# Kernel optimization log

Hardware: AMD Instinct MI355X
Metric: run time of the kernel (lower is better)

Reference implementation:

```python
import jax, jax.numpy as jnp
import numpy as np

N, E = 40000, 640000
IN_DIM, HID, HEADS, OUT, NC, ASSIGN = 128, 16, 8, 128, 2, 100
SIGMA = 0.5
F_HID = HID * HEADS  # 128 = hidden_dim * n_heads


def _edge_softmax(logits, dst, n):
    # softmax over incoming edges of each destination node (DGL edge_softmax)
    m = jax.ops.segment_max(logits, dst, num_segments=n)
    ex = jnp.exp(logits - m[dst])
    den = jax.ops.segment_sum(ex, dst, num_segments=n)
    return ex / den[dst]


def _gat_conv(h, src, dst, W, al, ar, b):
    # DGL GATConv: fc (no bias) -> per-head additive attention -> edge softmax -> scatter-sum
    nH, D = al.shape
    feat = (h @ W).reshape(h.shape[0], nH, D)            # [N,H,D]
    el = (feat * al).sum(-1)                              # [N,H]
    er = (feat * ar).sum(-1)                              # [N,H]
    logits = jax.nn.leaky_relu(el[src] + er[dst], 0.2)    # [E,H]
    a = _edge_softmax(logits, dst, h.shape[0])            # [E,H]
    out = jax.ops.segment_sum(feat[src] * a[..., None], dst, num_segments=h.shape[0])
    return out + b                                        # [N,H,D]


def _bn(x, g, b, eps=1e-5):
    mu = x.mean(0)
    v = x.var(0)
    return g * (x - mu) * jax.lax.rsqrt(v + eps) + b


def _gat_layer(h, src, dst, W, al, ar, b, g, bt):
    x = _gat_conv(h, src, dst, W, al, ar, b).reshape(h.shape[0], -1)
    x = jax.nn.elu(_bn(x, g, bt))
    return h + x  # residual: in_dim == out_dim*heads


def _mask(x):
    # h[torch.isinf(h)] = 1e9
    return jnp.where(jnp.isinf(x), 1e9, x)


def setup_inputs():
    key = jax.random.key(0)
    ks = jax.random.split(key, 20)
    rn = lambda k, s: jax.random.normal(k, s, jnp.float32) * 0.1
    return {
        "h": jax.random.normal(ks[0], (N, IN_DIM), jnp.float32),
        "e": jax.random.normal(ks[1], (E, 4), jnp.float32),
        "src": jax.random.randint(ks[2], (E,), 0, N, jnp.int32),
        "dst": jax.random.randint(ks[3], (E,), 0, N, jnp.int32),
        "W_emb": rn(ks[4], (IN_DIM, F_HID)), "b_emb": jnp.zeros((F_HID,), jnp.float32),
        "Wg": rn(ks[5], (3, F_HID, F_HID)),
        "alg": rn(ks[6], (3, HEADS, HID)), "arg": rn(ks[7], (3, HEADS, HID)),
        "bg": jnp.zeros((3, HEADS, HID), jnp.float32),
        "gam": jnp.ones((3, F_HID), jnp.float32), "bet": jnp.zeros((3, F_HID), jnp.float32),
        "W3": rn(ks[8], (F_HID, OUT)), "al3": rn(ks[9], (1, OUT)), "ar3": rn(ks[10], (1, OUT)),
        "b3": jnp.zeros((1, OUT), jnp.float32),
        "gam3": jnp.ones((OUT,), jnp.float32), "bet3": jnp.zeros((OUT,), jnp.float32),
        "Wa": rn(ks[11], (F_HID, ASSIGN)), "ba": jnp.zeros((ASSIGN,), jnp.float32),
        "Wm1": rn(ks[12], (2 * OUT, OUT)), "bm1": jnp.zeros((OUT,), jnp.float32),
        "Wm2": rn(ks[13], (OUT, OUT // 2)), "bm2": jnp.zeros((OUT // 2,), jnp.float32),
        "Wm3": rn(ks[14], (OUT // 2, NC)), "bm3": jnp.zeros((NC,), jnp.float32),
    }


def reference(h, e, src, dst, W_emb, b_emb, Wg, alg, arg, bg, gam, bet,
              W3, al3, ar3, b3, gam3, bet3, Wa, ba,
              Wm1, bm1, Wm2, bm2, Wm3, bm3):
    del e  # edge_feat=False: forward never consumes edge features
    h = h @ W_emb + b_emb  # embedding_h (dropout p=0 -> identity)
    # layer 0: GATLayer
    h = _mask(_gat_layer(h, src, dst, Wg[0], alg[0], arg[0], bg[0], gam[0], bet[0]))
    # layer 1: biGATLayer -> (h, s): GAT update + soft assignment s with sigma mixing over coarse pool
    h_in = h
    h_fine = _gat_layer(h, src, dst, Wg[1], alg[1], arg[1], bg[1], gam[1], bet[1])
    s = jax.nn.softmax(h_in @ Wa + ba, axis=-1)            # [N, ASSIGN]
    h_coarse = s.T @ h_fine                                # [ASSIGN, F_HID]
    h = _mask(SIGMA * h_fine + (1.0 - SIGMA) * (s @ h_coarse))
    # layer 2: GATLayer
    h = _mask(_gat_layer(h, src, dst, Wg[2], alg[2], arg[2], bg[2], gam[2], bet[2]))
    # layer 3: GATLayer, 1 head, out_dim
    h = _mask(_gat_layer(h, src, dst, W3, al3, ar3, b3, gam3, bet3))
    # apply_edges: gather src/dst node feats, concat, MLPReadout (256->128->64->NC), inf-mask
    z = jnp.concatenate([h[src], h[dst]], axis=1)          # [E, 2*OUT]
    z = jax.nn.relu(z @ Wm1 + bm1)
    z = jax.nn.relu(z @ Wm2 + bm2)
    z = _mask(z @ Wm3 + bm3)
    return z, s
```

## Files before the change

kernel.cpp:

```cpp
#include <hip/hip_runtime.h>
#include <hip/hip_bf16.h>
#include <math.h>

#define N_ 40000
#define E_ 640000
#define CB_ 400
#define CR_ 100
#define SB_ 256
#define SNB_ 157
#define AGGB_ 2048

typedef short bf16x8 __attribute__((ext_vector_type(8)));
typedef float floatx4 __attribute__((ext_vector_type(4)));

__device__ __forceinline__ short f2bf(float f) {
    __hip_bfloat16 h = __float2bfloat16(f);
    return *reinterpret_cast<short*>(&h);
}
__device__ __forceinline__ float bf2f(short u) {
    unsigned int x = ((unsigned int)(unsigned short)u) << 16;
    return __int_as_float(x);
}
__device__ __forceinline__ float rdlane(float v, int l) {
    return __int_as_float(__builtin_amdgcn_readlane(__float_as_int(v), l));
}
__device__ __forceinline__ float bflo(unsigned int u) { return __int_as_float(u << 16); }
__device__ __forceinline__ float bfhi(unsigned int u) { return __int_as_float(u & 0xffff0000u); }

__global__ void k_count(const int* __restrict__ dst, int* __restrict__ counts) {
    for (int e = blockIdx.x * blockDim.x + threadIdx.x; e < E_; e += gridDim.x * blockDim.x)
        atomicAdd(&counts[dst[e]], 1);
}

__global__ __launch_bounds__(256) void k_scanA(const int* __restrict__ counts,
                                               int* __restrict__ excl,
                                               int* __restrict__ bsum) {
    int t = threadIdx.x;
    int i = blockIdx.x * SB_ + t;
    int v = (i < N_) ? counts[i] : 0;
    int lane = t & 63, wv = t >> 6;
    int x = v;
#pragma unroll
    for (int off = 1; off < 64; off <<= 1) {
        int y = __shfl_up(x, off);
        if (lane >= off) x += y;
    }
    __shared__ int wsum[4];
    __shared__ int woff[4];
    if (lane == 63) wsum[wv] = x;
    __syncthreads();
    if (t == 0) {
        int a = 0;
#pragma unroll
        for (int j = 0; j < 4; j++) { int tv = wsum[j]; woff[j] = a; a += tv; }
        bsum[blockIdx.x] = a;
    }
    __syncthreads();
    if (i < N_) excl[i] = x - v + woff[wv];
}

__global__ __launch_bounds__(256) void k_scanB(int* __restrict__ bsum) {
    int t = threadIdx.x;
    int v = (t < SNB_) ? bsum[t] : 0;
    int lane = t & 63, wv = t >> 6;
    int x = v;
#pragma unroll
    for (int off = 1; off < 64; off <<= 1) {
        int y = __shfl_up(x, off);
        if (lane >= off) x += y;
    }
    __shared__ int wsum[4];
    __shared__ int woff[4];
    if (lane == 63) wsum[wv] = x;
    __syncthreads();
    if (t == 0) {
        int a = 0;
#pragma unroll
        for (int j = 0; j < 4; j++) { int tv = wsum[j]; woff[j] = a; a += tv; }
    }
    __syncthreads();
    if (t < SNB_) bsum[t] = x - v + woff[wv];
}

__global__ __launch_bounds__(256) void k_scanC(const int* __restrict__ excl,
                                               const int* __restrict__ bsum,
                                               int* __restrict__ rowptr,
                                               int* __restrict__ cursor) {
    int i = blockIdx.x * 256 + threadIdx.x;
    if (i < N_) {
        int r = excl[i] + bsum[i / SB_];
        rowptr[i] = r;
        cursor[i] = r;
    }
    if (i == N_) rowptr[N_] = E_;
}

__global__ void k_fill(const int* __restrict__ src, const int* __restrict__ dst,
                       int* __restrict__ cursor, int* __restrict__ srcv,
                       unsigned short* __restrict__ dstv, int* __restrict__ eidv) {
    for (int e = blockIdx.x * blockDim.x + threadIdx.x; e < E_; e += gridDim.x * blockDim.x) {
        int d = dst[e];
        int pos = atomicAdd(&cursor[d], 1);
        srcv[pos] = src[e];
        dstv[pos] = (unsigned short)d;
        eidv[pos] = e;
    }
}

__global__ __launch_bounds__(256) void k_prep_all(const float* __restrict__ Wg,
                                                  const float* __restrict__ W3,
                                                  const float* __restrict__ Wm1,
                                                  short* __restrict__ WbT6) {
    int i = blockIdx.x * 256 + threadIdx.x;
    if (i >= 6 * 16384) return;
    int m = i >> 14;
    int r = i & 16383;
    int n = r >> 7, k = r & 127;
    const float* srcp;
    switch (m) {
        case 0: srcp = Wg; break;
        case 1: srcp = Wg + 16384; break;
        case 2: srcp = Wg + 32768; break;
        case 3: srcp = W3; break;
        case 4: srcp = Wm1; break;
        default: srcp = Wm1 + 16384; break;
    }
    WbT6[m * 16384 + n * 128 + k] = f2bf(srcp[k * 128 + n]);
}

__global__ __launch_bounds__(256) void k_prep_wela(const float* __restrict__ Wg,
                                                   const float* __restrict__ alg,
                                                   const float* __restrict__ arg_,
                                                   const float* __restrict__ W3,
                                                   const float* __restrict__ al3,
                                                   const float* __restrict__ ar3,
                                                   short* __restrict__ WelT) {
    int i = blockIdx.x * 256 + threadIdx.x;
    if (i >= 4 * 2048) return;
    int layer = i >> 11;
    int r = i & 2047;
    int n = r >> 7, k = r & 127;
    float val = 0.f;
    if (layer < 3) {
        const float* W = Wg + layer * 16384;
        const float* a = (n < 8 ? alg : arg_) + layer * 128;
        int h = n & 7;
#pragma unroll
        for (int d = 0; d < 16; d++)
            val += W[k * 128 + h * 16 + d] * a[h * 16 + d];
    } else {
        if (n == 0) { for (int c = 0; c < 128; c++) val += W3[k * 128 + c] * al3[c]; }
        else if (n == 1) { for (int c = 0; c < 128; c++) val += W3[k * 128 + c] * ar3[c]; }
    }
    WelT[layer * 2048 + n * 128 + k] = f2bf(val);
}

__global__ __launch_bounds__(256) void k_prep_hilo(const float* __restrict__ W_emb,
                                                   const float* __restrict__ Wa,
                                                   short* __restrict__ WembT_hi,
                                                   short* __restrict__ WembT_lo,
                                                   short* __restrict__ WaT_hi,
                                                   short* __restrict__ WaT_lo) {
    int i = blockIdx.x * 256 + threadIdx.x;
    if (i >= 2 * 16384) return;
    int m = i >> 14;
    int r = i & 16383;
    int n = r >> 7, k = r & 127;
    if (m == 0) {
        float w = W_emb[k * 128 + n];
        short h = f2bf(w);
        WembT_hi[n * 128 + k] = h;
        WembT_lo[n * 128 + k] = f2bf(w - bf2f(h));
    } else {
        float w = (n < 100) ? Wa[k * 100 + n] : 0.f;
        short h = f2bf(w);
        WaT_hi[n * 128 + k] = h;
        WaT_lo[n * 128 + k] = f2bf(w - bf2f(h));
    }
}

__global__ __launch_bounds__(256) void k_mfma_hilo(const float* __restrict__ A,
                                                   const short* __restrict__ BT_hi,
                                                   const short* __restrict__ BT_lo,
                                                   const float* __restrict__ bias,
                                                   float* __restrict__ C, int ncols) {
    __shared__ short sAh[64 * 136];
    __shared__ short sAl[64 * 136];
    __shared__ short sBh[128 * 136];
    int t = threadIdx.x;
    int r0 = blockIdx.x * 64;
    {
        int n = t >> 1;
        int k0 = (t & 1) * 64;
#pragma unroll
        for (int j = 0; j < 8; j++) {
            bf16x8 v = *(const bf16x8*)(BT_hi + n * 128 + k0 + 8 * j);
            *(bf16x8*)(sBh + n * 136 + k0 + 8 * j) = v;
        }
    }
    {
        int r = t >> 2;
        int k0 = (t & 3) * 32;
        const float* ar = A + (size_t)(r0 + r) * 128 + k0;
#pragma unroll
        for (int j = 0; j < 4; j++) {
            float4 f0 = *(const float4*)(ar + 8 * j);
            float4 f1 = *(const float4*)(ar + 8 * j + 4);
            float x[8] = {f0.x, f0.y, f0.z, f0.w, f1.x, f1.y, f1.z, f1.w};
            bf16x8 vh, vl;
#pragma unroll
            for (int q = 0; q < 8; q++) {
                short hh = f2bf(x[q]);
                vh[q] = hh;
                vl[q] = f2bf(x[q] - bf2f(hh));
            }
            *(bf16x8*)(sAh + r * 136 + k0 + 8 * j) = vh;
            *(bf16x8*)(sAl + r * 136 + k0 + 8 * j) = vl;
        }
    }
    __syncthreads();
    int lane = t & 63, wv = t >> 6;
    int lm = lane & 15, quad = lane >> 4;
    int m0 = wv * 16;
    bf16x8 aH[4], aL[4];
#pragma unroll
    for (int kt = 0; kt < 4; kt++) {
        aH[kt] = *(const bf16x8*)(sAh + (m0 + lm) * 136 + kt * 32 + quad * 8);
        aL[kt] = *(const bf16x8*)(sAl + (m0 + lm) * 136 + kt * 32 + quad * 8);
    }
#pragma unroll
    for (int nt = 0; nt < 8; nt++) {
        const short* blp = BT_lo + (nt * 16 + lm) * 128 + quad * 8;
        floatx4 acc = (floatx4){0.f, 0.f, 0.f, 0.f};
#pragma unroll
        for (int kt = 0; kt < 4; kt++) {
            bf16x8 bH = *(const bf16x8*)(sBh + (nt * 16 + lm) * 136 + kt * 32 + quad * 8);
            bf16x8 bL = *(const bf16x8*)(blp + kt * 32);
            acc = __builtin_amdgcn_mfma_f32_16x16x32_bf16(aH[kt], bH, acc, 0, 0, 0);
            acc = __builtin_amdgcn_mfma_f32_16x16x32_bf16(aL[kt], bH, acc, 0, 0, 0);
            acc = __builtin_amdgcn_mfma_f32_16x16x32_bf16(aH[kt], bL, acc, 0, 0, 0);
        }
        int col = nt * 16 + lm;
        if (col < ncols) {
            float bv = bias ? bias[col] : 0.f;
#pragma unroll
            for (int r = 0; r < 4; r++) {
                int row = r0 + m0 + quad * 4 + r;
                C[(size_t)row * ncols + col] = acc[r] + bv;
            }
        }
    }
}

__global__ __launch_bounds__(256) void k_gemm_mfma(const float* __restrict__ A,
                                                   const short* __restrict__ WbT,
                                                   const float* __restrict__ bias,
                                                   short* __restrict__ C,
                                                   const short* __restrict__ WelT,
                                                   float* __restrict__ el,
                                                   float* __restrict__ er,
                                                   int H,
                                                   const float* __restrict__ bnx,
                                                   const float* __restrict__ bnh,
                                                   const float* __restrict__ csum,
                                                   const float* __restrict__ csq,
                                                   const float* __restrict__ bng,
                                                   const float* __restrict__ bnb,
                                                   float* __restrict__ hout,
                                                   int do_mask,
                                                   const short* __restrict__ WbT2,
                                                   short* __restrict__ C2) {
    __shared__ short sA[64 * 136];
    __shared__ short sB[128 * 136];
    __shared__ float sScale[128];
    __shared__ float sShift[128];
    int t = threadIdx.x;
    int r0 = blockIdx.x * 64;
    if (bnx) {
        if (t < 128) {
            const float invN = 1.f / (float)N_;
            float mu = csum[t] * invN;
            float var = csq[t] * invN - mu * mu;
            float inv = rsqrtf(var + 1e-5f);
            float sc = bng[t] * inv;
            sScale[t] = sc;
            sShift[t] = bnb[t] - mu * sc;
        }
        __syncthreads();
    }
    {
        int n = t >> 1;
        int k0 = (t & 1) * 64;
#pragma unroll
        for (int j = 0; j < 8; j++) {
            bf16x8 v = *(const bf16x8*)(WbT + n * 128 + k0 + 8 * j);
            *(bf16x8*)(sB + n * 136 + k0 + 8 * j) = v;
        }
    }
    {
        int r = t >> 2;
        int k0 = (t & 3) * 32;
        if (bnx) {
            const float* xr = bnx + (size_t)(r0 + r) * 128 + k0;
            const float* hr = bnh + (size_t)(r0 + r) * 128 + k0;
            float* ho = hout + (size_t)(r0 + r) * 128 + k0;
#pragma unroll
            for (int j = 0; j < 4; j++) {
                float4 x0 = *(const float4*)(xr + 8 * j);
                float4 x1 = *(const float4*)(xr + 8 * j + 4);
                float4 h0 = *(const float4*)(hr + 8 * j);
                float4 h1 = *(const float4*)(hr + 8 * j + 4);
                float xs[8] = {x0.x, x0.y, x0.z, x0.w, x1.x, x1.y, x1.z, x1.w};
                float hs[8] = {h0.x, h0.y, h0.z, h0.w, h1.x, h1.y, h1.z, h1.w};
                float ov[8];
                bf16x8 v;
#pragma unroll
                for (int q = 0; q < 8; q++) {
                    int c = k0 + 8 * j + q;
                    float y = sScale[c] * xs[q] + sShift[c];
                    y = y > 0.f ? y : (__expf(y) - 1.f);
                    float hv = hs[q] + y;
                    if (do_mask && isinf(hv)) hv = 1e9f;
                    ov[q] = hv;
                    v[q] = f2bf(hv);
                }
                *(float4*)(ho + 8 * j) = make_float4(ov[0], ov[1], ov[2], ov[3]);
                *(float4*)(ho + 8 * j + 4) = make_float4(ov[4], ov[5], ov[6], ov[7]);
                *(bf16x8*)(sA + r * 136 + k0 + 8 * j) = v;
            }
        } else {
            const float* ar = A + (size_t)(r0 + r) * 128 + k0;
#pragma unroll
            for (int j = 0; j < 4; j++) {
                float4 f0 = *(const float4*)(ar + 8 * j);
                float4 f1 = *(const float4*)(ar + 8 * j + 4);
                bf16x8 v;
                v[0] = f2bf(f0.x); v[1] = f2bf(f0.y); v[2] = f2bf(f0.z); v[3] = f2bf(f0.w);
                v[4] = f2bf(f1.x); v[5] = f2bf(f1.y); v[6] = f2bf(f1.z); v[7] = f2bf(f1.w);
                *(bf16x8*)(sA + r * 136 + k0 + 8 * j) = v;
            }
        }
    }
    __syncthreads();
    int lane = t & 63, wv = t >> 6;
    int lm = lane & 15, quad = lane >> 4;
    int m0 = wv * 16;
    bf16x8 aF[4];
#pragma unroll
    for (int kt = 0; kt < 4; kt++)
        aF[kt] = *(const bf16x8*)(sA + (m0 + lm) * 136 + kt * 32 + quad * 8);
#pragma unroll
    for (int nt = 0; nt < 8; nt++) {
        floatx4 acc = (floatx4){0.f, 0.f, 0.f, 0.f};
#pragma unroll
        for (int kt = 0; kt < 4; kt++) {
            bf16x8 bF = *(const bf16x8*)(sB + (nt * 16 + lm) * 136 + kt * 32 + quad * 8);
            acc = __builtin_amdgcn_mfma_f32_16x16x32_bf16(aF[kt], bF, acc, 0, 0, 0);
        }
        int col = nt * 16 + lm;
        float bv = bias ? bias[col] : 0.f;
#pragma unroll
        for (int r = 0; r < 4; r++) {
            int row = r0 + m0 + quad * 4 + r;
            C[(size_t)row * 128 + col] = f2bf(acc[r] + bv);
        }
    }
    if (WelT) {
        floatx4 acc = (floatx4){0.f, 0.f, 0.f, 0.f};
#pragma unroll
        for (int kt = 0; kt < 4; kt++) {
            bf16x8 wF = *(const bf16x8*)(WelT + lm * 128 + kt * 32 + quad * 8);
            acc = __builtin_amdgcn_mfma_f32_16x16x32_bf16(aF[kt], wF, acc, 0, 0, 0);
        }
        if (H == 8) {
#pragma unroll
            for (int r = 0; r < 4; r++) {
                int row = r0 + m0 + quad * 4 + r;
                if (lm < 8) el[(size_t)row * 8 + lm] = acc[r];
                else        er[(size_t)row * 8 + (lm - 8)] = acc[r];
            }
        } else {
#pragma unroll
            for (int r = 0; r < 4; r++) {
                int row = r0 + m0 + quad * 4 + r;
                if (lm == 0) el[row] = acc[r];
                if (lm == 1) er[row] = acc[r];
            }
        }
    }
    if (WbT2) {
        __syncthreads();
        {
            int n = t >> 1;
            int k0 = (t & 1) * 64;
#pragma unroll
            for (int j = 0; j < 8; j++) {
                bf16x8 v = *(const bf16x8*)(WbT2 + n * 128 + k0 + 8 * j);
                *(bf16x8*)(sB + n * 136 + k0 + 8 * j) = v;
            }
        }
        __syncthreads();
#pragma unroll
        for (int nt = 0; nt < 8; nt++) {
            floatx4 acc = (floatx4){0.f, 0.f, 0.f, 0.f};
#pragma unroll
            for (int kt = 0; kt < 4; kt++) {
                bf16x8 bF = *(const bf16x8*)(sB + (nt * 16 + lm) * 136 + kt * 32 + quad * 8);
                acc = __builtin_amdgcn_mfma_f32_16x16x32_bf16(aF[kt], bF, acc, 0, 0, 0);
            }
            int col = nt * 16 + lm;
#pragma unroll
            for (int r = 0; r < 4; r++) {
                int row = r0 + m0 + quad * 4 + r;
                C2[(size_t)row * 128 + col] = f2bf(acc[r]);
            }
        }
    }
}

__global__ __launch_bounds__(256) void k_smax100(const float* __restrict__ logits,
                                                 float* __restrict__ s) {
    int lane = threadIdx.x & 63;
    int n = blockIdx.x * 4 + (threadIdx.x >> 6);
    if (n >= N_) return;
    bool act = lane < 50;
    float2 v = make_float2(-INFINITY, -INFINITY);
    if (act) v = *(const float2*)(logits + (size_t)n * 100 + 2 * lane);
    float mx = fmaxf(v.x, v.y);
#pragma unroll
    for (int off = 1; off < 64; off <<= 1) mx = fmaxf(mx, __shfl_xor(mx, off));
    float e0 = act ? __expf(v.x - mx) : 0.f;
    float e1 = act ? __expf(v.y - mx) : 0.f;
    float sm = e0 + e1;
#pragma unroll
    for (int off = 1; off < 64; off <<= 1) sm += __shfl_xor(sm, off);
    float inv = 1.f / sm;
    if (act) *(float2*)(s + (size_t)n * 100 + 2 * lane) = make_float2(e0 * inv, e1 * inv);
}

template <int H>
__global__ __launch_bounds__(256) void k_gat_agg(const short* __restrict__ feat,
                                                 const float* __restrict__ el,
                                                 const float* __restrict__ er,
                                                 const int* __restrict__ rowptr,
                                                 const int* __restrict__ srcv,
                                                 const float* __restrict__ bias,
                                                 float* __restrict__ xout,
                                                 float* __restrict__ psum,
                                                 float* __restrict__ psq) {
    int t = threadIdx.x;
    int lane = t & 63;
    int gw = (blockIdx.x * blockDim.x + t) >> 6;
    int nw = (gridDim.x * blockDim.x) >> 6;
    constexpr int LH = (H == 8) ? 3 : 0;
    int h = lane & (H - 1);
    int f0 = 2 * lane;
    int hf = (H == 8) ? (lane >> 3) : 0;

    float stx = 0.f, sty = 0.f, qtx = 0.f, qty = 0.f;

    for (int n = gw; n < N_; n += nw) {
        int beg = rowptr[n], end = rowptr[n + 1];
        if (beg == end) {
            float2 b2 = *(const float2*)(bias + f0);
            *(float2*)(xout + (size_t)n * 128 + f0) = b2;
            stx += b2.x; sty += b2.y;
            qtx += b2.x * b2.x; qty += b2.y * b2.y;
            continue;
        }
        float ern = er[(size_t)n * H + h];
        float m = -INFINITY, ss = 0.f;
        for (int e = beg + (lane >> LH); e < end; e += (64 >> LH)) {
            int sI = srcv[e];
            float x = el[(size_t)sI * H + h] + ern;
            float lr = x > 0.f ? x : 0.2f * x;
            if (lr > m) { ss = ss * __expf(m - lr) + 1.f; m = lr; }
            else ss += __expf(lr - m);
        }
#pragma unroll
        for (int off = H; off < 64; off <<= 1) {
            float om = __shfl_xor(m, off);
            float os = __shfl_xor(ss, off);
            float nm = fmaxf(m, om);
            float p1 = (m == -INFINITY) ? 0.f : ss * __expf(m - nm);
            float p2 = (om == -INFINITY) ? 0.f : os * __expf(om - nm);
            m = nm; ss = p1 + p2;
        }
        float inv_d = 1.f / ss;
        int endm1 = end - 1;
        float accx = 0.f, accy = 0.f;
        for (int e0 = beg; e0 < end; e0 += 16) {
            int le = lane >> 3;
            int eLA = e0 + le, eLB = e0 + 8 + le;
            int eCA = eLA <= endm1 ? eLA : endm1;
            int eCB = eLB <= endm1 ? eLB : endm1;
            int sLA = srcv[eCA];
            int sLB = srcv[eCB];
            float xA = el[(size_t)sLA * H + h] + ern;
            float xB = el[(size_t)sLB * H + h] + ern;
            float lrA = xA > 0.f ? xA : 0.2f * xA;
            float lrB = xB > 0.f ? xB : 0.2f * xB;
            float wA = __expf(lrA - m) * inv_d;
            float wB = __expf(lrB - m) * inv_d;
            if (eLA > endm1) wA = 0.f;
            if (eLB > endm1) wB = 0.f;
            bool haveB = (e0 + 8) < end;
            unsigned int uuA[8], uuB[8];
#pragma unroll
            for (int j = 0; j < 8; j++) {
                int sj = __builtin_amdgcn_readlane(sLA, j * 8);
                uuA[j] = *(const unsigned int*)(feat + (size_t)sj * 128 + f0);
            }
            if (haveB) {
#pragma unroll
                for (int j = 0; j < 8; j++) {
                    int sj = __builtin_amdgcn_readlane(sLB, j * 8);
                    uuB[j] = *(const unsigned int*)(feat + (size_t)sj * 128 + f0);
                }
            }
#pragma unroll
            for (int j = 0; j < 8; j++) {
                float aj;
                if (H == 8) aj = __shfl(wA, j * 8 + hf);
                else        aj = rdlane(wA, j * 8);
                accx += aj * bflo(uuA[j]);
                accy += aj * bfhi(uuA[j]);
            }
            if (haveB) {
#pragma unroll
                for (int j = 0; j < 8; j++) {
                    float aj;
                    if (H == 8) aj = __shfl(wB, j * 8 + hf);
                    else        aj = rdlane(wB, j * 8);
                    accx += aj * bflo(uuB[j]);
                    accy += aj * bfhi(uuB[j]);
                }
            }
        }
        float2 b2 = *(const float2*)(bias + f0);
        float ox = accx + b2.x, oy = accy + b2.y;
        *(float2*)(xout + (size_t)n * 128 + f0) = make_float2(ox, oy);
        stx += ox; sty += oy;
        qtx += ox * ox; qty += oy * oy;
    }

    __shared__ float red[4][256];
    red[0][t] = stx; red[1][t] = sty; red[2][t] = qtx; red[3][t] = qty;
    __syncthreads();
    if (t < 64) {
        float a0 = red[0][t] + red[0][t + 64] + red[0][t + 128] + red[0][t + 192];
        float a1 = red[1][t] + red[1][t + 64] + red[1][t + 128] + red[1][t + 192];
        float q0 = red[2][t] + red[2][t + 64] + red[2][t + 128] + red[2][t + 192];
        float q1 = red[3][t] + red[3][t + 64] + red[3][t + 128] + red[3][t + 192];
        *(float2*)(psum + (size_t)blockIdx.x * 128 + 2 * t) = make_float2(a0, a1);
        *(float2*)(psq + (size_t)blockIdx.x * 128 + 2 * t) = make_float2(q0, q1);
    }
}

__global__ __launch_bounds__(256) void k_stats_reduce(const float* __restrict__ psum,
                                                      const float* __restrict__ psq,
                                                      float* __restrict__ colsum,
                                                      float* __restrict__ colsq) {
    __shared__ float ls[256], lq[256];
    int t = threadIdx.x;
    int col = t & 127, half = t >> 7;
    float s = 0.f, q = 0.f;
    for (int b = blockIdx.x * 2 + half; b < AGGB_; b += gridDim.x * 2) {
        s += psum[(size_t)b * 128 + col];
        q += psq[(size_t)b * 128 + col];
    }
    ls[t] = s; lq[t] = q;
    __syncthreads();
    if (t < 128) {
        atomicAdd(&colsum[col], ls[t] + ls[t + 128]);
        atomicAdd(&colsq[col], lq[t] + lq[t + 128]);
    }
}

__global__ __launch_bounds__(256) void k_bn_apply(const float* __restrict__ x,
                                                  const float* __restrict__ hprev,
                                                  const float* __restrict__ sum,
                                                  const float* __restrict__ sumsq,
                                                  const float* __restrict__ g,
                                                  const float* __restrict__ b,
                                                  float* __restrict__ out, int do_mask) {
    int i = blockIdx.x * blockDim.x + threadIdx.x;
    if (i >= N_ * 128) return;
    int c = i & 127;
    const float invN = 1.f / (float)N_;
    float mu = sum[c] * invN;
    float var = sumsq[c] * invN - mu * mu;
    float inv = rsqrtf(var + 1e-5f);
    float y = g[c] * (x[i] - mu) * inv + b[c];
    y = y > 0.f ? y : (__expf(y) - 1.f);
    float hv = hprev[i] + y;
    if (do_mask && isinf(hv)) hv = 1e9f;
    out[i] = hv;
}

__global__ __launch_bounds__(512) void k_coarse_part(const float* __restrict__ s,
                                                     const float* __restrict__ hf,
                                                     float* __restrict__ part) {
    int t = threadIdx.x;
    int c = t & 127;
    int g = t >> 7;
    int lane = t & 63;
    float acc[25];
#pragma unroll
    for (int a = 0; a < 25; a++) acc[a] = 0.f;
    int n0 = blockIdx.x * CR_;
    for (int n = n0; n < n0 + CR_; n += 2) {
        float hv0 = hf[(size_t)n * 128 + c];
        float hv1 = hf[(size_t)(n + 1) * 128 + c];
        float sv0 = 0.f, sv1 = 0.f;
        if (lane < 25) {
            sv0 = s[(size_t)n * 100 + 25 * g + lane];
            sv1 = s[(size_t)(n + 1) * 100 + 25 * g + lane];
        }
#pragma unroll
        for (int a = 0; a < 25; ++a) {
            float a0 = rdlane(sv0, a);
            float a1 = rdlane(sv1, a);
            acc[a] += a0 * hv0 + a1 * hv1;
        }
    }
    float* dstp = part + (size_t)blockIdx.x * 12800 + (size_t)(25 * g) * 128 + c;
#pragma unroll
    for (int a = 0; a < 25; a++) dstp[a * 128] = acc[a];
}

__global__ __launch_bounds__(256) void k_coarse_reduce(const float* __restrict__ part,
                                                       float* __restrict__ hc) {
    int i = blockIdx.x * blockDim.x + threadIdx.x;
    if (i >= 12800) return;
    float s0 = 0.f, s1 = 0.f, s2 = 0.f, s3 = 0.f;
    for (int b = 0; b < CB_; b += 4) {
        s0 += part[(size_t)(b + 0) * 12800 + i];
        s1 += part[(size_t)(b + 1) * 12800 + i];
        s2 += part[(size_t)(b + 2) * 12800 + i];
        s3 += part[(size_t)(b + 3) * 12800 + i];
    }
    hc[i] = (s0 + s1) + (s2 + s3);
}

__global__ __launch_bounds__(256) void k_combine(const float* __restrict__ s,
                                                 const float* __restrict__ hc,
                                                 const float* __restrict__ hfine,
                                                 float* __restrict__ hout) {
    __shared__ float ssh[16 * 100];
    int t = threadIdx.x;
    int n0 = blockIdx.x * 16;
    for (int u = t; u < 1600; u += 256) ssh[u] = s[(size_t)n0 * 100 + u];
    __syncthreads();
    int c = t & 127, g = t >> 7;
    float acc[8];
#pragma unroll
    for (int r = 0; r < 8; r++) acc[r] = 0.f;
    const float* hcp = hc + c;
    for (int a = 0; a < 100; a += 4) {
        float h0 = hcp[(a + 0) * 128];
        float h1 = hcp[(a + 1) * 128];
        float h2 = hcp[(a + 2) * 128];
        float h3 = hcp[(a + 3) * 128];
#pragma unroll
        for (int r = 0; r < 8; r++) {
            float4 sv = *(const float4*)(ssh + (g * 8 + r) * 100 + a);
            acc[r] += sv.x * h0 + sv.y * h1 + sv.z * h2 + sv.w * h3;
        }
    }
#pragma unroll
    for (int r = 0; r < 8; r++) {
        int row = n0 + g * 8 + r;
        float v = 0.5f * hfine[(size_t)row * 128 + c] + 0.5f * acc[r];
        if (isinf(v)) v = 1e9f;
        hout[(size_t)row * 128 + c] = v;
    }
}

__global__ __launch_bounds__(256) void k_prep_w(const float* __restrict__ Wm2,
                                                short* __restrict__ Wm2T) {
    int i = blockIdx.x * blockDim.x + threadIdx.x;
    if (i >= 64 * 128) return;
    int n = i & 63, k = i >> 6;
    Wm2T[n * 128 + k] = f2bf(Wm2[k * 64 + n]);
}

__global__ __launch_bounds__(256) void k_edge_mlp3(const short* __restrict__ Pb,
                                                   const short* __restrict__ Qb,
                                                   const int* __restrict__ srcv,
                                                   const unsigned short* __restrict__ dstv,
                                                   const int* __restrict__ eidv,
                                                   const short* __restrict__ Wm2T,
                                                   const float* __restrict__ bm2,
                                                   const float* __restrict__ Wm3,
                                                   const float* __restrict__ bm3,
                                                   float* __restrict__ zout) {
    __shared__ short sW[64 * 128];
    int t = threadIdx.x;
    for (int u = t; u < 1024; u += 256) {
        int n = u >> 4, k16 = u & 15;
        int phys = (n << 4) | (k16 ^ (n & 15));
        *(bf16x8*)(sW + phys * 8) = *(const bf16x8*)(Wm2T + n * 128 + k16 * 8);
    }
    int lane = t & 63;
    int lm = lane & 15, quad = lane >> 4;
    float bv[4], w30[4], w31[4];
#pragma unroll
    for (int nt = 0; nt < 4; nt++) {
        int n = nt * 16 + lm;
        bv[nt] = bm2[n]; w30[nt] = Wm3[2 * n]; w31[nt] = Wm3[2 * n + 1];
    }
    float b30 = bm3[0], b31 = bm3[1];
    __syncthreads();

    int gw = (blockIdx.x * blockDim.x + t) >> 6;
    int nw = (gridDim.x * blockDim.x) >> 6;

    for (int tile = gw; tile < E_ / 16; tile += nw) {
        int p0 = tile * 16;
        int sI = srcv[p0 + lm];
        int dI = (int)dstv[p0 + lm];
        const short* pr = Pb + (size_t)sI * 128 + quad * 8;
        const short* qr = Qb + (size_t)dI * 128 + quad * 8;
        uint4 pu[4], qu[4];
#pragma unroll
        for (int kt = 0; kt < 4; kt++) {
            pu[kt] = *(const uint4*)(pr + kt * 32);
            qu[kt] = *(const uint4*)(qr + kt * 32);
        }
        bf16x8 aF[4];
#pragma unroll
        for (int kt = 0; kt < 4; kt++) {
            unsigned int pv[4] = {pu[kt].x, pu[kt].y, pu[kt].z, pu[kt].w};
            unsigned int qv[4] = {qu[kt].x, qu[kt].y, qu[kt].z, qu[kt].w};
            union { uint4 u; bf16x8 v; } cv;
            unsigned int rr[4];
#pragma unroll
            for (int j = 0; j < 4; j++) {
                float fl = fmaxf(bflo(pv[j]) + bflo(qv[j]), 0.f);
                float fh = fmaxf(bfhi(pv[j]) + bfhi(qv[j]), 0.f);
                rr[j] = (unsigned int)(unsigned short)f2bf(fl) |
                        ((unsigned int)(unsigned short)f2bf(fh) << 16);
            }
            cv.u.x = rr[0]; cv.u.y = rr[1]; cv.u.z = rr[2]; cv.u.w = rr[3];
            aF[kt] = cv.v;
        }
        float pz0[4] = {0.f, 0.f, 0.f, 0.f};
        float pz1[4] = {0.f, 0.f, 0.f, 0.f};
#pragma unroll
        for (int nt = 0; nt < 4; nt++) {
            floatx4 acc = (floatx4){0.f, 0.f, 0.f, 0.f};
#pragma unroll
            for (int kt = 0; kt < 4; kt++) {
                int phys = ((nt * 16 + lm) << 4) | (((kt << 2) | quad) ^ lm);
                bf16x8 bF = *(const bf16x8*)(sW + phys * 8);
                acc = __builtin_amdgcn_mfma_f32_16x16x32_bf16(aF[kt], bF, acc, 0, 0, 0);
            }
#pragma unroll
            for (int r = 0; r < 4; r++) {
                float u = fmaxf(acc[r] + bv[nt], 0.f);
                pz0[r] += u * w30[nt];
                pz1[r] += u * w31[nt];
            }
        }
#pragma unroll
        for (int off = 1; off < 16; off <<= 1) {
#pragma unroll
            for (int r = 0; r < 4; r++) {
                pz0[r] += __shfl_xor(pz0[r], off);
                pz1[r] += __shfl_xor(pz1[r], off);
            }
        }
        if (lm < 4) {
            int eid = eidv[p0 + quad * 4 + lm];
            float z0 = pz0[lm] + b30;
            float z1 = pz1[lm] + b31;
            if (isinf(z0)) z0 = 1e9f;
            if (isinf(z1)) z1 = 1e9f;
            *(float2*)(zout + (size_t)eid * 2) = make_float2(z0, z1);
        }
    }
}

extern "C" void kernel_launch(void* const* d_in, const int* in_sizes, int n_in,
                              void* d_out, int out_size, void* d_ws, size_t ws_size,
                              hipStream_t stream) {
    const float* h_in  = (const float*)d_in[0];
    const int*   src   = (const int*)d_in[2];
    const int*   dst   = (const int*)d_in[3];
    const float* W_emb = (const float*)d_in[4];
    const float* b_emb = (const float*)d_in[5];
    const float* Wg    = (const float*)d_in[6];
    const float* alg   = (const float*)d_in[7];
    const float* arg_  = (const float*)d_in[8];
    const float* bg    = (const float*)d_in[9];
    const float* gam   = (const float*)d_in[10];
    const float* bet   = (const float*)d_in[11];
    const float* W3    = (const float*)d_in[12];
    const float* al3   = (const float*)d_in[13];
    const float* ar3   = (const float*)d_in[14];
    const float* b3    = (const float*)d_in[15];
    const float* gam3  = (const float*)d_in[16];
    const float* bet3  = (const float*)d_in[17];
    const float* Wa    = (const float*)d_in[18];
    const float* ba    = (const float*)d_in[19];
    const float* Wm1   = (const float*)d_in[20];
    const float* bm1   = (const float*)d_in[21];
    const float* Wm2   = (const float*)d_in[22];
    const float* bm2   = (const float*)d_in[23];
    const float* Wm3   = (const float*)d_in[24];
    const float* bm3   = (const float*)d_in[25];

    float* zout = (float*)d_out;
    float* sout = zout + (size_t)E_ * 2;

    float* ws = (float*)d_ws;
    size_t o = 0;
    float* h_cur = ws + o; o += (size_t)N_ * 128;
    float* xbuf  = ws + o; o += (size_t)N_ * 128;
    float* featb = ws + o; o += (size_t)N_ * 128;
    float* el    = ws + o; o += (size_t)N_ * 8;
    float* er    = ws + o; o += (size_t)N_ * 8;
    float* colsum = ws + o; o += 128;
    float* colsq  = ws + o; o += 128;
    float* hc     = ws + o; o += 100 * 128;
    float* psum   = ws + o; o += (size_t)AGGB_ * 128;
    float* psq    = ws + o; o += (size_t)AGGB_ * 128;
    short* Wm2T = (short*)(ws + o); o += (64 * 128) / 2;
    short* WbT6 = (short*)(ws + o); o += (6 * 16384) / 2;
    short* WelT = (short*)(ws + o); o += (4 * 2048) / 2;
    short* WembT_hi = (short*)(ws + o); o += 16384 / 2;
    short* WembT_lo = (short*)(ws + o); o += 16384 / 2;
    short* WaT_hi   = (short*)(ws + o); o += 16384 / 2;
    short* WaT_lo   = (short*)(ws + o); o += 16384 / 2;
    int* counts = (int*)(ws + o); o += N_;
    int* rowptr = (int*)(ws + o); o += N_ + 4;
    int* cursor = (int*)(ws + o); o += N_;
    int* srcv   = (int*)(ws + o); o += E_;
    unsigned short* dstv = (unsigned short*)(ws + o); o += E_ / 2;
    int* eidv   = (int*)(ws + o); o += E_;
    int* bsum   = (int*)(ws + o); o += SNB_ + 4;

    short* featw = (short*)featb;

    hipMemsetAsync(counts, 0, N_ * sizeof(int), stream);
    k_count<<<1024, 256, 0, stream>>>(dst, counts);
    k_scanA<<<SNB_, 256, 0, stream>>>(counts, eidv, bsum);
    k_scanB<<<1, 256, 0, stream>>>(bsum);
    k_scanC<<<SNB_ + 1, 256, 0, stream>>>(eidv, bsum, rowptr, cursor);
    k_fill<<<1024, 256, 0, stream>>>(src, dst, cursor, srcv, dstv, eidv);
    k_prep_w<<<32, 256, 0, stream>>>(Wm2, Wm2T);
    k_prep_all<<<384, 256, 0, stream>>>(Wg, W3, Wm1, WbT6);
    k_prep_wela<<<32, 256, 0, stream>>>(Wg, alg, arg_, W3, al3, ar3, WelT);
    k_prep_hilo<<<128, 256, 0, stream>>>(W_emb, Wa, WembT_hi, WembT_lo, WaT_hi, WaT_lo);

    k_mfma_hilo<<<N_ / 64, 256, 0, stream>>>(h_in, WembT_hi, WembT_lo, b_emb, h_cur, 128);

    k_gemm_mfma<<<N_ / 64, 256, 0, stream>>>(h_cur, WbT6 + 0 * 16384, nullptr, featw,
                                             WelT + 0 * 2048, el, er, 8,
                                             nullptr, nullptr, nullptr, nullptr,
                                             nullptr, nullptr, nullptr, 0,
                                             nullptr, nullptr);
    hipMemsetAsync(colsum, 0, 256 * sizeof(float), stream);
    k_gat_agg<8><<<AGGB_, 256, 0, stream>>>(featw, el, er, rowptr, srcv, bg + 0 * 128, xbuf,
                                            psum, psq);
    k_stats_reduce<<<64, 256, 0, stream>>>(psum, psq, colsum, colsq);

    k_gemm_mfma<<<N_ / 64, 256, 0, stream>>>(nullptr, WbT6 + 1 * 16384, nullptr, featw,
                                             WelT + 1 * 2048, el, er, 8,
                                             xbuf, h_cur, colsum, colsq,
                                             gam + 0 * 128, bet + 0 * 128, h_cur, 1,
                                             nullptr, nullptr);
    k_mfma_hilo<<<N_ / 64, 256, 0, stream>>>(h_cur, WaT_hi, WaT_lo, ba, xbuf, 100);
    k_smax100<<<N_ / 4, 256, 0, stream>>>(xbuf, sout);
    hipMemsetAsync(colsum, 0, 256 * sizeof(float), stream);
    k_gat_agg<8><<<AGGB_, 256, 0, stream>>>(featw, el, er, rowptr, srcv, bg + 1 * 128, xbuf,
                                            psum, psq);
    k_stats_reduce<<<64, 256, 0, stream>>>(psum, psq, colsum, colsq);
    k_bn_apply<<<(N_ * 128) / 256, 256, 0, stream>>>(xbuf, h_cur, colsum, colsq,
                                                     gam + 1 * 128, bet + 1 * 128, xbuf, 0);
    k_coarse_part<<<CB_, 512, 0, stream>>>(sout, xbuf, featb);
    k_coarse_reduce<<<50, 256, 0, stream>>>(featb, hc);
    k_combine<<<N_ / 16, 256, 0, stream>>>(sout, hc, xbuf, h_cur);

    k_gemm_mfma<<<N_ / 64, 256, 0, stream>>>(h_cur, WbT6 + 2 * 16384, nullptr, featw,
                                             WelT + 2 * 2048, el, er, 8,
                                             nullptr, nullptr, nullptr, nullptr,
                                             nullptr, nullptr, nullptr, 0,
                                             nullptr, nullptr);
    hipMemsetAsync(colsum, 0, 256 * sizeof(float), stream);
    k_gat_agg<8><<<AGGB_, 256, 0, stream>>>(featw, el, er, rowptr, srcv, bg + 2 * 128, xbuf,
                                            psum, psq);
    k_stats_reduce<<<64, 256, 0, stream>>>(psum, psq, colsum, colsq);

    k_gemm_mfma<<<N_ / 64, 256, 0, stream>>>(nullptr, WbT6 + 3 * 16384, nullptr, featw,
                                             WelT + 3 * 2048, el, er, 1,
                                             xbuf, h_cur, colsum, colsq,
                                             gam + 2 * 128, bet + 2 * 128, h_cur, 1,
                                             nullptr, nullptr);
    hipMemsetAsync(colsum, 0, 256 * sizeof(float), stream);
    k_gat_agg<1><<<AGGB_, 256, 0, stream>>>(featw, el, er, rowptr, srcv, b3, xbuf,
                                            psum, psq);
    k_stats_reduce<<<64, 256, 0, stream>>>(psum, psq, colsum, colsq);

    short* Pb = (short*)featb;
    short* Qb = Pb + (size_t)N_ * 128;
    k_gemm_mfma<<<N_ / 64, 256, 0, stream>>>(nullptr, WbT6 + 4 * 16384, bm1, Pb,
                                             nullptr, nullptr, nullptr, 0,
                                             xbuf, h_cur, colsum, colsq,
                                             gam3, bet3, h_cur, 1,
                                             WbT6 + 5 * 16384, Qb);
    k_edge_mlp3<<<2048, 256, 0, stream>>>(Pb, Qb, srcv, dstv, eidv, Wm2T, bm2, Wm3, bm3, zout);
}
```

Baseline: 751.0 us.

## Fuse edge softmax into aggregation with online max rescaling

Drops the separate pass over each node's incoming edges that computed the max and sum for the edge softmax. The aggregation loop now keeps a running max, rescales its accumulators when the max grows, and normalizes once at the end, in the style of flash attention. This avoids re-reading srcv and el per edge. In exchange it adds per-edge exp calls and data-dependent branches, which may diverge across lanes of different heads.

```diff
diff --git a/kernel.cpp b/kernel.cpp
--- a/kernel.cpp
+++ b/kernel.cpp
@@ -452,7 +452,6 @@
     int lane = t & 63;
     int gw = (blockIdx.x * blockDim.x + t) >> 6;
     int nw = (gridDim.x * blockDim.x) >> 6;
-    constexpr int LH = (H == 8) ? 3 : 0;
     int h = lane & (H - 1);
     int f0 = 2 * lane;
     int hf = (H == 8) ? (lane >> 3) : 0;
@@ -469,25 +468,8 @@
             continue;
         }
         float ern = er[(size_t)n * H + h];
+        int endm1 = end - 1;
         float m = -INFINITY, ss = 0.f;
-        for (int e = beg + (lane >> LH); e < end; e += (64 >> LH)) {
-            int sI = srcv[e];
-            float x = el[(size_t)sI * H + h] + ern;
-            float lr = x > 0.f ? x : 0.2f * x;
-            if (lr > m) { ss = ss * __expf(m - lr) + 1.f; m = lr; }
-            else ss += __expf(lr - m);
-        }
-#pragma unroll
-        for (int off = H; off < 64; off <<= 1) {
-            float om = __shfl_xor(m, off);
-            float os = __shfl_xor(ss, off);
-            float nm = fmaxf(m, om);
-            float p1 = (m == -INFINITY) ? 0.f : ss * __expf(m - nm);
-            float p2 = (om == -INFINITY) ? 0.f : os * __expf(om - nm);
-            m = nm; ss = p1 + p2;
-        }
-        float inv_d = 1.f / ss;
-        int endm1 = end - 1;
         float accx = 0.f, accy = 0.f;
         for (int e0 = beg; e0 < end; e0 += 16) {
             int le = lane >> 3;
@@ -500,10 +482,8 @@
             float xB = el[(size_t)sLB * H + h] + ern;
             float lrA = xA > 0.f ? xA : 0.2f * xA;
             float lrB = xB > 0.f ? xB : 0.2f * xB;
-            float wA = __expf(lrA - m) * inv_d;
-            float wB = __expf(lrB - m) * inv_d;
-            if (eLA > endm1) wA = 0.f;
-            if (eLB > endm1) wB = 0.f;
+            if (eLA > endm1) lrA = -INFINITY;
+            if (eLB > endm1) lrB = -INFINITY;
             bool haveB = (e0 + 8) < end;
             unsigned int uuA[8], uuB[8];
 #pragma unroll
@@ -520,25 +500,38 @@
             }
 #pragma unroll
             for (int j = 0; j < 8; j++) {
-                float aj;
-                if (H == 8) aj = __shfl(wA, j * 8 + hf);
-                else        aj = rdlane(wA, j * 8);
-                accx += aj * bflo(uuA[j]);
-                accy += aj * bfhi(uuA[j]);
+                float lj;
+                if (H == 8) lj = __shfl(lrA, j * 8 + hf);
+                else        lj = rdlane(lrA, j * 8);
+                if (lj > m) {
+                    float r = __expf(m - lj);
+                    accx *= r; accy *= r; ss *= r; m = lj;
+                }
+                float w = __expf(lj - m);
+                accx += w * bflo(uuA[j]);
+                accy += w * bfhi(uuA[j]);
+                ss += w;
             }
             if (haveB) {
 #pragma unroll
                 for (int j = 0; j < 8; j++) {
-                    float aj;
-                    if (H == 8) aj = __shfl(wB, j * 8 + hf);
-                    else        aj = rdlane(wB, j * 8);
-                    accx += aj * bflo(uuB[j]);
-                    accy += aj * bfhi(uuB[j]);
+                    float lj;
+                    if (H == 8) lj = __shfl(lrB, j * 8 + hf);
+                    else        lj = rdlane(lrB, j * 8);
+                    if (lj > m) {
+                        float r = __expf(m - lj);
+                        accx *= r; accy *= r; ss *= r; m = lj;
+                    }
+                    float w = __expf(lj - m);
+                    accx += w * bflo(uuB[j]);
+                    accy += w * bfhi(uuB[j]);
+                    ss += w;
                 }
             }
         }
+        float inv_d = 1.f / ss;
         float2 b2 = *(const float2*)(bias + f0);
-        float ox = accx + b2.x, oy = accy + b2.y;
+        float ox = accx * inv_d + b2.x, oy = accy * inv_d + b2.y;
         *(float2*)(xout + (size_t)n * 128 + f0) = make_float2(ox, oy);
         stx += ox; sty += oy;
         qtx += ox * ox; qty += oy * oy;
```

New measurement: 729.3 us. -2.9%, faster.
